# Kernel tuning notes

Hardware: AMD Instinct MI355X
Metric: run time of the kernel (lower is better)

The kernel has to match this reference:

```python
import jax, jax.numpy as jnp
import numpy as np

B, S, D = 4, 2048, 1024
THETA = 10000.0


def apply_rope(x, pos):
    # x: (..., seq, d), pos: (..., seq). Interleaved-pair rotary embedding.
    d = x.shape[-1]
    inv_freq = 1.0 / (THETA ** (jnp.arange(0, d, 2, dtype=jnp.float32) / d))  # (d/2,)
    ang = pos.astype(jnp.float32)[..., None] * inv_freq                        # (..., seq, d/2)
    cos, sin = jnp.cos(ang), jnp.sin(ang)
    x1, x2 = x[..., 0::2], x[..., 1::2]
    r1 = x1 * cos - x2 * sin
    r2 = x1 * sin + x2 * cos
    return jnp.stack([r1, r2], axis=-1).reshape(x.shape)


def setup_inputs() -> dict:
    key = jax.random.key(0)
    ks = jax.random.split(key, 5)
    scale = 1.0 / np.sqrt(D)
    x = jax.random.normal(ks[0], (B, S, D), dtype=jnp.float32)
    Wq = jax.random.normal(ks[1], (D, D), dtype=jnp.float32) * scale
    Wk = jax.random.normal(ks[2], (D, D), dtype=jnp.float32) * scale
    Wv = jax.random.normal(ks[3], (D, D), dtype=jnp.float32) * scale
    Wo = jax.random.normal(ks[4], (D, D), dtype=jnp.float32) * scale
    token_positions = jnp.tile(jnp.arange(S, dtype=jnp.int64), (B, 1))
    return {"x": x, "Wq": Wq, "Wk": Wk, "Wv": Wv, "Wo": Wo,
            "token_positions": token_positions}


def reference(x, Wq, Wk, Wv, Wo, token_positions):
    # Projections (Linear stores W as (out, in); y = x @ W^T, no bias)
    Q = x @ Wq.T
    K = x @ Wk.T
    V = x @ Wv.T
    Q = apply_rope(Q, token_positions)
    K = apply_rope(K, token_positions)
    d_k = K.shape[-1]
    scores = jnp.einsum('bqd,bkd->bqk', Q, K) / jnp.sqrt(jnp.float32(d_k))
    seq = x.shape[-2]
    causal = jnp.tril(jnp.ones((seq, seq), dtype=bool))  # qi >= kj
    scores = jnp.where(causal, scores, -jnp.inf)
    weights = jax.nn.softmax(scores, axis=-1)
    attn = jnp.einsum('bqk,bkd->bqd', weights, V)
    return attn @ Wo.T
```

## Files before the change

kernel.cpp:

```cpp
#include <hip/hip_runtime.h>
#include <math.h>

constexpr int Bc = 4;
constexpr int Sc = 2048;
constexpr int Dc = 1024;

using bf16x8 = __bf16 __attribute__((ext_vector_type(8)));
using f32x4  = float  __attribute__((ext_vector_type(4)));

__device__ __forceinline__ ushort f2bf(float f) {
    uint u = __float_as_uint(f);
    u += 0x7FFFu + ((u >> 16) & 1u);
    return (ushort)(u >> 16);
}
__device__ __forceinline__ float bf2f(ushort h) {
    return __uint_as_float(((uint)h) << 16);
}

__device__ __forceinline__ void gload_lds16(const void* g, void* l) {
    __builtin_amdgcn_global_load_lds(
        (const __attribute__((address_space(1))) void*)g,
        (__attribute__((address_space(3))) void*)l, 16, 0, 0);
}

__global__ __launch_bounds__(256)
void cvt_f32_bf16_k(const float* __restrict__ src, ushort* __restrict__ dst, int n)
{
    for (long i = ((long)blockIdx.x * 256 + threadIdx.x) * 4; i < n;
         i += (long)gridDim.x * 256 * 4) {
        float4 v = *(const float4*)(src + i);
        ushort4 o;
        o.x = f2bf(v.x); o.y = f2bf(v.y); o.z = f2bf(v.z); o.w = f2bf(v.w);
        *(ushort4*)(dst + i) = o;
    }
}

enum { M_BF16 = 0, M_ROPE = 1, M_SCORES = 2, M_PV = 3, M_F32OUT = 4, M_VTRANS = 5 };

template<int MODE>
__global__ __launch_bounds__(256)
void mfma_bt_k(const ushort* __restrict__ A, const ushort* __restrict__ B,
               void* __restrict__ Cv, int M, int N, int K,
               long sA, long sB, long sC)
{
    const int bx = blockIdx.x, by = blockIdx.y, bz = blockIdx.z;
    if (MODE == M_SCORES && bx > by) return;

    A += (long)bz * sA;
    B += (long)bz * sB;

    __shared__ ushort As[128][32];
    __shared__ ushort Bs[128][32];

    const int t    = threadIdx.x;
    const int lane = t & 63;
    const int wid  = t >> 6;
    const int wr   = wid >> 1;
    const int wc   = wid & 1;

    const int srow = wid * 32 + (lane >> 2);
    const int scol = (lane & 3) * 8;
    const long abase = (long)(by * 128) * K;
    const long bbase = (long)(bx * 128) * K;

    f32x4 acc[4][4];
#pragma unroll
    for (int m = 0; m < 4; ++m)
#pragma unroll
        for (int n = 0; n < 4; ++n) acc[m][n] = (f32x4){0.f, 0.f, 0.f, 0.f};

    const int kend = (MODE == M_PV) ? min(K, (by + 1) * 128) : K;

    const int fr = lane & 15;
    const int fk = (lane >> 4) * 8;

    for (int k0 = 0; k0 < kend; k0 += 32) {
        __syncthreads();
#pragma unroll
        for (int c = 0; c < 2; ++c) {
            const int r = srow + c * 16;
            gload_lds16(A + abase + (long)r * K + k0 + scol,
                        &As[wid * 32 + c * 16][0]);
            gload_lds16(B + bbase + (long)r * K + k0 + scol,
                        &Bs[wid * 32 + c * 16][0]);
        }
        __syncthreads();

        bf16x8 af[4], bfr[4];
#pragma unroll
        for (int m = 0; m < 4; ++m)
            af[m] = *(const bf16x8*)&As[wr * 64 + m * 16 + fr][fk];
#pragma unroll
        for (int n = 0; n < 4; ++n)
            bfr[n] = *(const bf16x8*)&Bs[wc * 64 + n * 16 + fr][fk];
#pragma unroll
        for (int m = 0; m < 4; ++m)
#pragma unroll
            for (int n = 0; n < 4; ++n)
                acc[m][n] = __builtin_amdgcn_mfma_f32_16x16x32_bf16(
                    af[m], bfr[n], acc[m][n], 0, 0, 0);
    }

    if constexpr (MODE == M_VTRANS) {
        __shared__ ushort Ts[128][136];
#pragma unroll
        for (int m = 0; m < 4; ++m)
#pragma unroll
            for (int n = 0; n < 4; ++n)
#pragma unroll
                for (int j = 0; j < 4; ++j) {
                    const int c_loc = wc * 64 + n * 16 + fr;
                    const int r_loc = wr * 64 + m * 16 + (lane >> 4) * 4 + j;
                    Ts[c_loc][r_loc] = f2bf(acc[m][n][j]);
                }
        __syncthreads();
        const int b  = (by * 128) >> 11;
        const int s0 = (by * 128) & (Sc - 1);
        ushort* Vt = (ushort*)Cv + (long)b * Dc * Sc;
#pragma unroll
        for (int pass = 0; pass < 8; ++pass) {
            const int ci = pass * 16 + (t >> 4);
            const int ch = t & 15;
            uint4 vv = *(const uint4*)&Ts[ci][ch * 8];
            *(uint4*)&Vt[(long)(bx * 128 + ci) * Sc + s0 + ch * 8] = vv;
        }
        return;
    }

    const int orow = by * 128 + wr * 64;
    const int ocol = bx * 128 + wc * 64;
#pragma unroll
    for (int m = 0; m < 4; ++m) {
#pragma unroll
        for (int n = 0; n < 4; ++n) {
            const int col = ocol + n * 16 + fr;
#pragma unroll
            for (int j = 0; j < 4; ++j) {
                const int row = orow + m * 16 + (lane >> 4) * 4 + j;
                float v = acc[m][n][j];
                if (MODE == M_SCORES) v *= 0.03125f;
                if (MODE == M_ROPE) {
                    float partner = __shfl_xor(v, 1);
                    const float kfac = 9.210340371976184f / 1024.0f;
                    float freq = expf(-(float)(col & ~1) * kfac);
                    float pos  = (float)(row & (Sc - 1));
                    float s, c;
                    sincosf(pos * freq, &s, &c);
                    v = (col & 1) ? fmaf(partner, s, v * c)
                                  : fmaf(-partner, s, v * c);
                }
                if (MODE == M_F32OUT) {
                    ((float*)Cv)[(long)bz * sC + (long)row * N + col] = v;
                } else {
                    ((ushort*)Cv)[(long)bz * sC + (long)row * N + col] = f2bf(v);
                }
            }
        }
    }
}

__device__ __forceinline__ float blk_reduce(float v, bool is_max, float* sm)
{
#pragma unroll
    for (int off = 32; off; off >>= 1) {
        float o = __shfl_down(v, off);
        v = is_max ? fmaxf(v, o) : (v + o);
    }
    const int lane = threadIdx.x & 63, wid = threadIdx.x >> 6;
    if (lane == 0) sm[wid] = v;
    __syncthreads();
    if (threadIdx.x == 0) {
        float r = sm[0];
        for (int w = 1; w < 4; ++w) r = is_max ? fmaxf(r, sm[w]) : (r + sm[w]);
        sm[0] = r;
    }
    __syncthreads();
    float r = sm[0];
    __syncthreads();
    return r;
}

__global__ __launch_bounds__(256)
void softmax_bf16_k(ushort* __restrict__ P, int seq)
{
    const int q = blockIdx.x, b = blockIdx.y;
    ushort* row = P + ((long)b * seq + q) * seq;
    const int valid = q + 1;
    const int t = threadIdx.x;
    __shared__ float buf[Sc];
    __shared__ float sm[4];

    for (int i = t; i < valid; i += 256) buf[i] = bf2f(row[i]);
    __syncthreads();

    float m = -1e30f;
    for (int i = t; i < valid; i += 256) m = fmaxf(m, buf[i]);
    m = blk_reduce(m, true, sm);

    float s = 0.0f;
    for (int i = t; i < valid; i += 256) {
        float e = __expf(buf[i] - m);
        buf[i] = e;
        s += e;
    }
    s = blk_reduce(s, false, sm);
    const float inv = 1.0f / s;

    for (int i = t; i < seq; i += 256)
        row[i] = (i < valid) ? f2bf(buf[i] * inv) : (ushort)0;
}

extern "C" void kernel_launch(void* const* d_in, const int* in_sizes, int n_in,
                              void* d_out, int out_size, void* d_ws, size_t ws_size,
                              hipStream_t stream)
{
    const float* x  = (const float*)d_in[0];
    const float* Wq = (const float*)d_in[1];
    const float* Wk = (const float*)d_in[2];
    const float* Wv = (const float*)d_in[3];
    const float* Wo = (const float*)d_in[4];
    float* out = (float*)d_out;

    const long MD = (long)Bc * Sc * Dc;
    const long DD = (long)Dc * Dc;

    ushort* Xb  = (ushort*)d_ws;
    ushort* Wqb = Xb  + MD;
    ushort* Wkb = Wqb + DD;
    ushort* Wvb = Wkb + DD;
    ushort* Wob = Wvb + DD;
    ushort* Qb  = Wob + DD;
    ushort* Kb  = Qb  + MD;
    ushort* Vt  = Kb  + MD;
    ushort* Pb  = Vt  + MD;
    ushort* Ab  = Pb  + (long)Bc * Sc * Sc;

    dim3 blk(256);

    cvt_f32_bf16_k<<<2048, blk, 0, stream>>>(x,  Xb,  (int)MD);
    cvt_f32_bf16_k<<<1024, blk, 0, stream>>>(Wq, Wqb, (int)DD);
    cvt_f32_bf16_k<<<1024, blk, 0, stream>>>(Wk, Wkb, (int)DD);
    cvt_f32_bf16_k<<<1024, blk, 0, stream>>>(Wv, Wvb, (int)DD);
    cvt_f32_bf16_k<<<1024, blk, 0, stream>>>(Wo, Wob, (int)DD);

    const int Mall = Bc * Sc;

    dim3 gproj(Dc / 128, Mall / 128, 1);
    mfma_bt_k<M_ROPE>  <<<gproj, blk, 0, stream>>>(Xb, Wqb, Qb, Mall, Dc, Dc, 0, 0, 0);
    mfma_bt_k<M_ROPE>  <<<gproj, blk, 0, stream>>>(Xb, Wkb, Kb, Mall, Dc, Dc, 0, 0, 0);
    mfma_bt_k<M_VTRANS><<<gproj, blk, 0, stream>>>(Xb, Wvb, Vt, Mall, Dc, Dc, 0, 0, 0);

    dim3 gsc(Sc / 128, Sc / 128, Bc);
    mfma_bt_k<M_SCORES><<<gsc, blk, 0, stream>>>(
        Qb, Kb, Pb, Sc, Sc, Dc, (long)Sc * Dc, (long)Sc * Dc, (long)Sc * Sc);

    dim3 gsm(Sc, Bc, 1);
    softmax_bf16_k<<<gsm, blk, 0, stream>>>(Pb, Sc);

    dim3 gpv(Dc / 128, Sc / 128, Bc);
    mfma_bt_k<M_PV><<<gpv, blk, 0, stream>>>(
        Pb, Vt, Ab, Sc, Dc, Sc, (long)Sc * Sc, (long)Dc * Sc, (long)Sc * Dc);

    mfma_bt_k<M_F32OUT><<<gproj, blk, 0, stream>>>(Ab, Wob, out, Mall, Dc, Dc, 0, 0, 0);
}
```

Baseline: 679.5 us.

## Fuse QKV projections, batch weight casts, and use wave-per-row register softmax

Merges the Q, K and V projection GEMMs into one launch, selecting the weight and epilogue (RoPE or transposed V store) by block column, and converts all four weights in a single kernel. Replaces the block-per-row shared-memory softmax with one wavefront per row that keeps 32 values per lane in registers and uses shuffle reductions. This removes launches and block barriers, and gives one bigger grid for better tail utilization. The fused kernel always reserves the transpose staging buffer in shared memory, which may lower occupancy for the Q/K blocks.

After: 1.043 ms. 1.53x slower.

```diff
diff --git a/kernel.cpp b/kernel.cpp
--- a/kernel.cpp
+++ b/kernel.cpp
@@ -35,7 +35,144 @@
     }
 }
 
-enum { M_BF16 = 0, M_ROPE = 1, M_SCORES = 2, M_PV = 3, M_F32OUT = 4, M_VTRANS = 5 };
+__global__ __launch_bounds__(256)
+void cvt_w4_k(const float* __restrict__ w0, const float* __restrict__ w1,
+              const float* __restrict__ w2, const float* __restrict__ w3,
+              ushort* __restrict__ o0, ushort* __restrict__ o1,
+              ushort* __restrict__ o2, ushort* __restrict__ o3)
+{
+    const long DD = 1L << 20;
+    const long tot = 4 * DD;
+    for (long i = ((long)blockIdx.x * 256 + threadIdx.x) * 4; i < tot;
+         i += (long)gridDim.x * 1024) {
+        const int sel = (int)(i >> 20);
+        const long off = i & (DD - 1);
+        const float* s = (sel == 0) ? w0 : (sel == 1) ? w1 : (sel == 2) ? w2 : w3;
+        ushort*      d = (sel == 0) ? o0 : (sel == 1) ? o1 : (sel == 2) ? o2 : o3;
+        float4 v = *(const float4*)(s + off);
+        ushort4 o;
+        o.x = f2bf(v.x); o.y = f2bf(v.y); o.z = f2bf(v.z); o.w = f2bf(v.w);
+        *(ushort4*)(d + off) = o;
+    }
+}
+
+__global__ __launch_bounds__(256)
+void mfma_qkv_k(const ushort* __restrict__ X,
+                const ushort* __restrict__ Wq, const ushort* __restrict__ Wk,
+                const ushort* __restrict__ Wv,
+                ushort* __restrict__ Qo, ushort* __restrict__ Ko,
+                ushort* __restrict__ Vt)
+{
+    const int bx = blockIdx.x, by = blockIdx.y;
+    const int sel = bx >> 3;
+    const int nx  = bx & 7;
+    const ushort* __restrict__ Wp = (sel == 0) ? Wq : (sel == 1) ? Wk : Wv;
+    const int K = Dc;
+
+    __shared__ ushort As[128][32];
+    __shared__ ushort Bs[128][32];
+    __shared__ ushort Ts[128][136];
+
+    const int t    = threadIdx.x;
+    const int lane = t & 63;
+    const int wid  = t >> 6;
+    const int wr   = wid >> 1;
+    const int wc   = wid & 1;
+
+    const int srow = wid * 32 + (lane >> 2);
+    const int scol = (lane & 3) * 8;
+    const long abase = (long)(by * 128) * K;
+    const long bbase = (long)(nx * 128) * K;
+
+    f32x4 acc[4][4];
+#pragma unroll
+    for (int m = 0; m < 4; ++m)
+#pragma unroll
+        for (int n = 0; n < 4; ++n) acc[m][n] = (f32x4){0.f, 0.f, 0.f, 0.f};
+
+    const int fr = lane & 15;
+    const int fk = (lane >> 4) * 8;
+
+    for (int k0 = 0; k0 < K; k0 += 32) {
+        __syncthreads();
+#pragma unroll
+        for (int c = 0; c < 2; ++c) {
+            const int r = srow + c * 16;
+            gload_lds16(X  + abase + (long)r * K + k0 + scol,
+                        &As[wid * 32 + c * 16][0]);
+            gload_lds16(Wp + bbase + (long)r * K + k0 + scol,
+                        &Bs[wid * 32 + c * 16][0]);
+        }
+        __syncthreads();
+
+        bf16x8 af[4], bfr[4];
+#pragma unroll
+        for (int m = 0; m < 4; ++m)
+            af[m] = *(const bf16x8*)&As[wr * 64 + m * 16 + fr][fk];
+#pragma unroll
+        for (int n = 0; n < 4; ++n)
+            bfr[n] = *(const bf16x8*)&Bs[wc * 64 + n * 16 + fr][fk];
+#pragma unroll
+        for (int m = 0; m < 4; ++m)
+#pragma unroll
+            for (int n = 0; n < 4; ++n)
+                acc[m][n] = __builtin_amdgcn_mfma_f32_16x16x32_bf16(
+                    af[m], bfr[n], acc[m][n], 0, 0, 0);
+    }
+
+    if (sel == 2) {
+        __syncthreads();
+#pragma unroll
+        for (int m = 0; m < 4; ++m)
+#pragma unroll
+            for (int n = 0; n < 4; ++n)
+#pragma unroll
+                for (int j = 0; j < 4; ++j) {
+                    const int c_loc = wc * 64 + n * 16 + fr;
+                    const int r_loc = wr * 64 + m * 16 + (lane >> 4) * 4 + j;
+                    Ts[c_loc][r_loc] = f2bf(acc[m][n][j]);
+                }
+        __syncthreads();
+        const int b  = by >> 4;
+        const int s0 = (by * 128) & (Sc - 1);
+        ushort* Vp = Vt + (long)b * Dc * Sc;
+#pragma unroll
+        for (int pass = 0; pass < 8; ++pass) {
+            const int ci = pass * 16 + (t >> 4);
+            const int ch = t & 15;
+            uint4 vv = *(const uint4*)&Ts[ci][ch * 8];
+            *(uint4*)&Vp[(long)(nx * 128 + ci) * Sc + s0 + ch * 8] = vv;
+        }
+        return;
+    }
+
+    ushort* C = (sel == 0) ? Qo : Ko;
+    const int orow = by * 128 + wr * 64;
+    const int ocol = nx * 128 + wc * 64;
+#pragma unroll
+    for (int m = 0; m < 4; ++m) {
+#pragma unroll
+        for (int n = 0; n < 4; ++n) {
+            const int col = ocol + n * 16 + fr;
+#pragma unroll
+            for (int j = 0; j < 4; ++j) {
+                const int row = orow + m * 16 + (lane >> 4) * 4 + j;
+                float v = acc[m][n][j];
+                float partner = __shfl_xor(v, 1);
+                const float kfac = 9.210340371976184f / 1024.0f;
+                float freq = expf(-(float)(col & ~1) * kfac);
+                float pos  = (float)(row & (Sc - 1));
+                float s, c;
+                sincosf(pos * freq, &s, &c);
+                v = (col & 1) ? fmaf(partner, s, v * c)
+                              : fmaf(-partner, s, v * c);
+                C[(long)row * Dc + col] = f2bf(v);
+            }
+        }
+    }
+}
+
+enum { M_SCORES = 2, M_PV = 3, M_F32OUT = 4 };
 
 template<int MODE>
 __global__ __launch_bounds__(256)
@@ -101,32 +238,6 @@
                     af[m], bfr[n], acc[m][n], 0, 0, 0);
     }
 
-    if constexpr (MODE == M_VTRANS) {
-        __shared__ ushort Ts[128][136];
-#pragma unroll
-        for (int m = 0; m < 4; ++m)
-#pragma unroll
-            for (int n = 0; n < 4; ++n)
-#pragma unroll
-                for (int j = 0; j < 4; ++j) {
-                    const int c_loc = wc * 64 + n * 16 + fr;
-                    const int r_loc = wr * 64 + m * 16 + (lane >> 4) * 4 + j;
-                    Ts[c_loc][r_loc] = f2bf(acc[m][n][j]);
-                }
-        __syncthreads();
-        const int b  = (by * 128) >> 11;
-        const int s0 = (by * 128) & (Sc - 1);
-        ushort* Vt = (ushort*)Cv + (long)b * Dc * Sc;
-#pragma unroll
-        for (int pass = 0; pass < 8; ++pass) {
-            const int ci = pass * 16 + (t >> 4);
-            const int ch = t & 15;
-            uint4 vv = *(const uint4*)&Ts[ci][ch * 8];
-            *(uint4*)&Vt[(long)(bx * 128 + ci) * Sc + s0 + ch * 8] = vv;
-        }
-        return;
-    }
-
     const int orow = by * 128 + wr * 64;
     const int ocol = bx * 128 + wc * 64;
 #pragma unroll
@@ -139,16 +250,6 @@
                 const int row = orow + m * 16 + (lane >> 4) * 4 + j;
                 float v = acc[m][n][j];
                 if (MODE == M_SCORES) v *= 0.03125f;
-                if (MODE == M_ROPE) {
-                    float partner = __shfl_xor(v, 1);
-                    const float kfac = 9.210340371976184f / 1024.0f;
-                    float freq = expf(-(float)(col & ~1) * kfac);
-                    float pos  = (float)(row & (Sc - 1));
-                    float s, c;
-                    sincosf(pos * freq, &s, &c);
-                    v = (col & 1) ? fmaf(partner, s, v * c)
-                                  : fmaf(-partner, s, v * c);
-                }
                 if (MODE == M_F32OUT) {
                     ((float*)Cv)[(long)bz * sC + (long)row * N + col] = v;
                 } else {
@@ -159,55 +260,53 @@
     }
 }
 
-__device__ __forceinline__ float blk_reduce(float v, bool is_max, float* sm)
-{
-#pragma unroll
-    for (int off = 32; off; off >>= 1) {
-        float o = __shfl_down(v, off);
-        v = is_max ? fmaxf(v, o) : (v + o);
-    }
-    const int lane = threadIdx.x & 63, wid = threadIdx.x >> 6;
-    if (lane == 0) sm[wid] = v;
-    __syncthreads();
-    if (threadIdx.x == 0) {
-        float r = sm[0];
-        for (int w = 1; w < 4; ++w) r = is_max ? fmaxf(r, sm[w]) : (r + sm[w]);
-        sm[0] = r;
-    }
-    __syncthreads();
-    float r = sm[0];
-    __syncthreads();
-    return r;
-}
-
-__global__ __launch_bounds__(256)
-void softmax_bf16_k(ushort* __restrict__ P, int seq)
-{
-    const int q = blockIdx.x, b = blockIdx.y;
-    ushort* row = P + ((long)b * seq + q) * seq;
+__global__ __launch_bounds__(256)
+void softmax_wave_k(ushort* __restrict__ P)
+{
+    const int t = threadIdx.x, lane = t & 63, w = t >> 6;
+    const long rowid = (long)blockIdx.x * 4 + w;
+    const int q = (int)(rowid & (Sc - 1));
+    ushort* row = P + rowid * Sc;
     const int valid = q + 1;
-    const int t = threadIdx.x;
-    __shared__ float buf[Sc];
-    __shared__ float sm[4];
-
-    for (int i = t; i < valid; i += 256) buf[i] = bf2f(row[i]);
-    __syncthreads();
-
+
+    float v[32];
     float m = -1e30f;
-    for (int i = t; i < valid; i += 256) m = fmaxf(m, buf[i]);
-    m = blk_reduce(m, true, sm);
-
-    float s = 0.0f;
-    for (int i = t; i < valid; i += 256) {
-        float e = __expf(buf[i] - m);
-        buf[i] = e;
-        s += e;
-    }
-    s = blk_reduce(s, false, sm);
+#pragma unroll
+    for (int c = 0; c < 4; ++c) {
+        uint4 raw = *(const uint4*)&row[c * 512 + lane * 8];
+        const ushort* rs = (const ushort*)&raw;
+#pragma unroll
+        for (int j = 0; j < 8; ++j) {
+            const int col = c * 512 + lane * 8 + j;
+            float f = bf2f(rs[j]);
+            v[c * 8 + j] = f;
+            if (col < valid) m = fmaxf(m, f);
+        }
+    }
+#pragma unroll
+    for (int off = 32; off; off >>= 1) m = fmaxf(m, __shfl_xor(m, off));
+
+    float s = 0.f;
+#pragma unroll
+    for (int c = 0; c < 4; ++c)
+#pragma unroll
+        for (int j = 0; j < 8; ++j) {
+            const int col = c * 512 + lane * 8 + j;
+            float e = (col < valid) ? __expf(v[c * 8 + j] - m) : 0.f;
+            v[c * 8 + j] = e;
+            s += e;
+        }
+#pragma unroll
+    for (int off = 32; off; off >>= 1) s += __shfl_xor(s, off);
     const float inv = 1.0f / s;
 
-    for (int i = t; i < seq; i += 256)
-        row[i] = (i < valid) ? f2bf(buf[i] * inv) : (ushort)0;
+#pragma unroll
+    for (int c = 0; c < 4; ++c) {
+        ushort o[8];
+#pragma unroll
+        for (int j = 0; j < 8; ++j) o[j] = f2bf(v[c * 8 + j] * inv);
+        *(uint4*)&row[c * 512 + lane * 8] = *(const uint4*)o;
+    }
 }
 
 extern "C" void kernel_launch(void* const* d_in, const int* in_sizes, int n_in,
@@ -237,29 +336,23 @@
 
     dim3 blk(256);
 
-    cvt_f32_bf16_k<<<2048, blk, 0, stream>>>(x,  Xb,  (int)MD);
-    cvt_f32_bf16_k<<<1024, blk, 0, stream>>>(Wq, Wqb, (int)DD);
-    cvt_f32_bf16_k<<<1024, blk, 0, stream>>>(Wk, Wkb, (int)DD);
-    cvt_f32_bf16_k<<<1024, blk, 0, stream>>>(Wv, Wvb, (int)DD);
-    cvt_f32_bf16_k<<<1024, blk, 0, stream>>>(Wo, Wob, (int)DD);
-
-    const int Mall = Bc * Sc;
-
-    dim3 gproj(Dc / 128, Mall / 128, 1);
-    mfma_bt_k<M_ROPE>  <<<gproj, blk, 0, stream>>>(Xb, Wqb, Qb, Mall, Dc, Dc, 0, 0, 0);
-    mfma_bt_k<M_ROPE>  <<<gproj, blk, 0, stream>>>(Xb, Wkb, Kb, Mall, Dc, Dc, 0, 0, 0);
-    mfma_bt_k<M_VTRANS><<<gproj, blk, 0, stream>>>(Xb, Wvb, Vt, Mall, Dc, Dc, 0, 0, 0);
+    cvt_f32_bf16_k<<<2048, blk, 0, stream>>>(x, Xb, (int)MD);
+    cvt_w4_k<<<4096, blk, 0, stream>>>(Wq, Wk, Wv, Wo, Wqb, Wkb, Wvb, Wob);
+
+    dim3 gqkv(24, 64, 1);
+    mfma_qkv_k<<<gqkv, blk, 0, stream>>>(Xb, Wqb, Wkb, Wvb, Qb, Kb, Vt);
 
     dim3 gsc(Sc / 128, Sc / 128, Bc);
     mfma_bt_k<M_SCORES><<<gsc, blk, 0, stream>>>(
         Qb, Kb, Pb, Sc, Sc, Dc, (long)Sc * Dc, (long)Sc * Dc, (long)Sc * Sc);
 
-    dim3 gsm(Sc, Bc, 1);
-    softmax_bf16_k<<<gsm, blk, 0, stream>>>(Pb, Sc);
+    softmax_wave_k<<<2048, blk, 0, stream>>>(Pb);
 
     dim3 gpv(Dc / 128, Sc / 128, Bc);
     mfma_bt_k<M_PV><<<gpv, blk, 0, stream>>>(
         Pb, Vt, Ab, Sc, Dc, Sc, (long)Sc * Sc, (long)Dc * Sc, (long)Sc * Dc);
 
-    mfma_bt_k<M_F32OUT><<<gproj, blk, 0, stream>>>(Ab, Wob, out, Mall, Dc, Dc, 0, 0, 0);
-}
+    dim3 gout(Dc / 128, (Bc * Sc) / 128, 1);
+    mfma_bt_k<M_F32OUT><<<gout, blk, 0, stream>>>(
+        Ab, Wob, out, Bc * Sc, Dc, Dc, 0, 0, 0);
+}
```
